# Kernel tuning notes

Measured on AMD Instinct MI355X. Metric: run time of the kernel, lower is better.

The kernel has to match this reference:

```python
import jax, jax.numpy as jnp
import numpy as np

DIM = 1024
RANK = 16
CLAMP = 5.0
PLASTICITY = 0.5
SING_THRESH = 0.8
SING_STRENGTH = 10.0


def setup_inputs() -> dict:
    key = jax.random.key(0)
    ks = jax.random.split(key, 8)
    B, S = 8, 4096
    v = jax.random.normal(ks[0], (B, S, DIM), dtype=jnp.float32)
    x = jax.random.normal(ks[1], (B, S, DIM), dtype=jnp.float32)
    U = jax.random.normal(ks[2], (DIM, RANK), dtype=jnp.float32) * 0.001
    W = jax.random.normal(ks[3], (DIM, RANK), dtype=jnp.float32) * 0.001
    # V: Linear(dim, 1, bias=False); init zeros in code, use small randn for coverage
    V_w = jax.random.normal(ks[4], (1, DIM), dtype=jnp.float32) * 0.01
    gate_w = jax.random.normal(ks[5], (DIM, DIM), dtype=jnp.float32) * 0.001
    gate_b = jnp.full((DIM,), 2.0, dtype=jnp.float32)
    forget_w = jax.random.normal(ks[6], (DIM, DIM), dtype=jnp.float32) * 0.01
    forget_b = jnp.full((DIM,), -3.0, dtype=jnp.float32)
    return {"v": v, "x": x, "U": U, "W": W, "V_w": V_w,
            "gate_w": gate_w, "gate_b": gate_b,
            "forget_w": forget_w, "forget_b": forget_b}


def reference(v, x, U, W, V_w, gate_w, gate_b, forget_w, forget_b):
    # Low-rank quadratic form: Gamma(v, v)
    proj = jnp.einsum('bsd,dr->bsr', v, U)                     # [B,S,R]
    norm = jnp.linalg.norm(proj, axis=-1, keepdims=True)       # [B,S,1]
    scale = 1.0 / (1.0 + norm)
    sq = proj * proj * scale                                   # [B,S,R]
    gamma = jnp.einsum('bsr,dr->bsd', sq, W)                   # [B,S,D]

    # Potential modulation (V has no bias)
    potential = jax.nn.sigmoid(jnp.einsum('bsd,od->bso', x, V_w))  # [B,S,1]
    gamma = gamma * (1.0 + potential)
    gamma = jnp.clip(gamma, -CLAMP, CLAMP)

    # Gate
    gate = jax.nn.sigmoid(jnp.einsum('bsd,ed->bse', x, gate_w) + gate_b)
    gamma = gamma * gate

    # Friction / damping
    friction = jax.nn.sigmoid(jnp.einsum('bsd,ed->bse', x, forget_w) + forget_b)
    out = gamma + friction * v

    # Reactive curvature (plasticity on kinetic energy)
    energy = jnp.tanh(jnp.mean(v * v, axis=-1, keepdims=True))
    out = out * (1.0 + PLASTICITY * energy)

    # Logical singularities (black holes)
    is_sing = (potential > SING_THRESH).astype(out.dtype)
    sing_mult = 1.0 + is_sing * (SING_STRENGTH - 1.0)
    out = out * sing_mult
    return out
```

## Files before the change

kernel.cpp:

```cpp
#include <hip/hip_runtime.h>
#include <hip/hip_fp16.h>
#include <math.h>


#define NROWS 32768
#define DIMD  1024

typedef float    f32x4 __attribute__((ext_vector_type(4)));
typedef _Float16 f16x8 __attribute__((ext_vector_type(8)));
typedef _Float16 f16x4 __attribute__((ext_vector_type(4)));

__global__ __launch_bounds__(256)
void k0_convert_w(const float* __restrict__ gw, const float* __restrict__ fw,
                  __half* __restrict__ wh) {
    const int NG = (2 * 1024 * 1024) / 4;
    for (int g = blockIdx.x * blockDim.x + threadIdx.x; g < NG; g += gridDim.x * blockDim.x) {
        int idx = g * 4;
        const float* src = (idx < 1024 * 1024) ? (gw + idx) : (fw + (idx - 1024 * 1024));
        f32x4 s = *(const f32x4*)src;
        f16x4 h;
        h[0] = (_Float16)s[0]; h[1] = (_Float16)s[1];
        h[2] = (_Float16)s[2]; h[3] = (_Float16)s[3];
        *(f16x4*)(wh + idx) = h;
    }
}

__global__ __launch_bounds__(256)
void k1_rowstats(const float* __restrict__ v, const float* __restrict__ x,
                 const float* __restrict__ U, const float* __restrict__ Vw,
                 float* __restrict__ sq_o, float* __restrict__ pot_o,
                 float* __restrict__ mult_o) {
    __shared__ float Us[1024][20];
    __shared__ float Vws[1024];
    const int tid = threadIdx.x;
    #pragma unroll
    for (int c = 0; c < 4; ++c) {
        int d = tid + 256 * c;
        const float* ur = U + (size_t)d * 16;
        *(f32x4*)&Us[d][0]  = *(const f32x4*)(ur);
        *(f32x4*)&Us[d][4]  = *(const f32x4*)(ur + 4);
        *(f32x4*)&Us[d][8]  = *(const f32x4*)(ur + 8);
        *(f32x4*)&Us[d][12] = *(const f32x4*)(ur + 12);
        Vws[d] = Vw[d];
    }
    __syncthreads();
    const int lane = tid & 63, wave = tid >> 6;
    const int gwv = blockIdx.x * 4 + wave;
    for (int rr = 0; rr < 8; ++rr) {
        int row = gwv + rr * 4096;
        const float* vr = v + (size_t)row * DIMD;
        const float* xr = x + (size_t)row * DIMD;
        float en = 0.f, pt = 0.f;
        float pr[16];
        #pragma unroll
        for (int r = 0; r < 16; ++r) pr[r] = 0.f;
        #pragma unroll 4
        for (int c = 0; c < 16; ++c) {
            int d = lane + 64 * c;
            float vv = vr[d];
            float xx = xr[d];
            en = fmaf(vv, vv, en);
            pt = fmaf(xx, Vws[d], pt);
            const float* up = &Us[d][0];
            #pragma unroll
            for (int r = 0; r < 16; ++r) pr[r] = fmaf(vv, up[r], pr[r]);
        }
        #pragma unroll
        for (int off = 32; off >= 1; off >>= 1) {
            en += __shfl_xor(en, off, 64);
            pt += __shfl_xor(pt, off, 64);
            #pragma unroll
            for (int r = 0; r < 16; ++r) pr[r] += __shfl_xor(pr[r], off, 64);
        }
        if (lane == 0) {
            float n2 = 0.f;
            #pragma unroll
            for (int r = 0; r < 16; ++r) n2 = fmaf(pr[r], pr[r], n2);
            float scale = 1.f / (1.f + sqrtf(n2));
            float p = 1.f / (1.f + expf(-pt));
            float energy = tanhf(en * (1.f / 1024.f));
            float mu = (1.f + 0.5f * energy) * (p > 0.8f ? 10.f : 1.f);
            float* sqr = sq_o + (size_t)row * 16;
            #pragma unroll
            for (int r = 0; r < 16; ++r) sqr[r] = pr[r] * pr[r] * scale;
            pot_o[row] = p;
            mult_o[row] = mu;
        }
    }
}

__global__ __launch_bounds__(256)
void k2_main(const float* __restrict__ x, const float* __restrict__ v,
             const __half* __restrict__ wh,
             const float* __restrict__ W, const float* __restrict__ gate_b,
             const float* __restrict__ forget_b, const float* __restrict__ sq_i,
             const float* __restrict__ pot_i, const float* __restrict__ mult_i,
             float* __restrict__ out) {
    __shared__ __half As[128][72];
    __shared__ __half Bs[2][64][64];
    __shared__ float  sqs[128][16];
    __shared__ float  Ws[64][20];
    __shared__ float  pots[128];
    __shared__ float  mults[128];
    __shared__ float  gbs[64];
    __shared__ float  fbs[64];

    const int tid  = threadIdx.x;
    const int lane = tid & 63, wave = tid >> 6;
    const int nt = blockIdx.x, mt = blockIdx.y;
    const int m0 = mt * 128, n0 = nt * 64;
    const int wm = (wave >> 1) * 64, wn = (wave & 1) * 32;

    {
        int r = tid >> 1, h = tid & 1;
        const float* s = sq_i + (size_t)(m0 + r) * 16 + h * 8;
        *(f32x4*)&sqs[r][h * 8]     = *(const f32x4*)(s);
        *(f32x4*)&sqs[r][h * 8 + 4] = *(const f32x4*)(s + 4);
        if (tid < 128) { pots[tid] = pot_i[m0 + tid]; mults[tid] = mult_i[m0 + tid]; }
        if (tid < 64)  { gbs[tid] = gate_b[n0 + tid]; fbs[tid] = forget_b[n0 + tid]; }
        int wr_ = tid >> 2, wq = tid & 3;
        *(f32x4*)&Ws[wr_][wq * 4] = *(const f32x4*)(W + (size_t)(n0 + wr_) * 16 + wq * 4);
    }

    f32x4 acc[2][4][2];
    #pragma unroll
    for (int a = 0; a < 2; ++a)
        #pragma unroll
        for (int m = 0; m < 4; ++m)
            #pragma unroll
            for (int n = 0; n < 2; ++n)
                acc[a][m][n] = (f32x4){0.f, 0.f, 0.f, 0.f};

    const int bn = lane >> 3;
    const int bs = (lane & 7) ^ bn;
    const int mat = wave >> 1;
    const __half* wsrc = wh + (size_t)(mat * 1024 + n0) * 1024;

    const int ar = tid >> 4;
    const int ac = tid & 15;
    const float* xbase = x + (size_t)(m0 + ar) * 1024 + ac * 4;

    for (int kt = 0; kt < 16; ++kt) {
        #pragma unroll
        for (int cc = 0; cc < 4; ++cc) {
            int c = (wave & 1) * 4 + cc;
            const __half* g = wsrc + (size_t)(c * 8 + bn) * 1024 + kt * 64 + bs * 8;
            __builtin_amdgcn_global_load_lds(
                (const __attribute__((address_space(1))) void*)g,
                (__attribute__((address_space(3))) void*)&Bs[mat][c * 8][0],
                16, 0, 0);
        }
        const float* xk = xbase + kt * 64;
        f32x4 xa[8];
        #pragma unroll
        for (int p = 0; p < 8; ++p) xa[p] = *(const f32x4*)(xk + (size_t)p * 16 * 1024);
        #pragma unroll
        for (int p = 0; p < 8; ++p) {
            f16x4 h;
            h[0] = (_Float16)xa[p][0]; h[1] = (_Float16)xa[p][1];
            h[2] = (_Float16)xa[p][2]; h[3] = (_Float16)xa[p][3];
            *(f16x4*)&As[p * 16 + ar][ac * 4] = h;
        }
        __syncthreads();

        #pragma unroll
        for (int kk = 0; kk < 2; ++kk) {
            f16x8 af[4];
            #pragma unroll
            for (int m = 0; m < 4; ++m) {
                int row = wm + m * 16 + (lane & 15);
                af[m] = *(const f16x8*)((const __half*)&As[row][0] + (lane >> 4) * 8 + kk * 32);
            }
            f16x8 bf[2][2];
            #pragma unroll
            for (int n = 0; n < 2; ++n) {
                int brow = wn + n * 16 + (lane & 15);
                int slot = ((lane >> 4) + kk * 4) ^ (brow & 7);
                bf[0][n] = *(const f16x8*)&Bs[0][brow][slot * 8];
                bf[1][n] = *(const f16x8*)&Bs[1][brow][slot * 8];
            }
            #pragma unroll
            for (int m = 0; m < 4; ++m)
                #pragma unroll
                for (int n = 0; n < 2; ++n) {
                    acc[0][m][n] = __builtin_amdgcn_mfma_f32_16x16x32_f16(af[m], bf[0][n], acc[0][m][n], 0, 0, 0);
                    acc[1][m][n] = __builtin_amdgcn_mfma_f32_16x16x32_f16(af[m], bf[1][n], acc[1][m][n], 0, 0, 0);
                }
        }
        __syncthreads();
    }

    const int cl = lane & 15;
    const int rq = lane >> 4;
    float gb2[2], fb2[2];
    f32x4 Wf[2][4];
    #pragma unroll
    for (int n = 0; n < 2; ++n) {
        int c = wn + n * 16 + cl;
        #pragma unroll
        for (int q = 0; q < 4; ++q) Wf[n][q] = *(const f32x4*)&Ws[c][q * 4];
        gb2[n] = gbs[c]; fb2[n] = fbs[c];
    }
    #pragma unroll
    for (int m = 0; m < 4; ++m) {
        #pragma unroll
        for (int i = 0; i < 4; ++i) {
            int rl = wm + m * 16 + rq * 4 + i;
            size_t gm = (size_t)(m0 + rl);
            f32x4 sr[4];
            #pragma unroll
            for (int q = 0; q < 4; ++q) sr[q] = *(const f32x4*)&sqs[rl][q * 4];
            float ptl = pots[rl], mu = mults[rl];
            float onep = 1.f + ptl;
            #pragma unroll
            for (int n = 0; n < 2; ++n) {
                float gamma = 0.f;
                #pragma unroll
                for (int q = 0; q < 4; ++q)
                    #pragma unroll
                    for (int j = 0; j < 4; ++j)
                        gamma = fmaf(sr[q][j], Wf[n][q][j], gamma);
                int gn = n0 + wn + n * 16 + cl;
                float gl = acc[0][m][n][i] + gb2[n];
                float fl = acc[1][m][n][i] + fb2[n];
                float gate = 1.f / (1.f + __expf(-gl));
                float fric = 1.f / (1.f + __expf(-fl));
                float gam = gamma * onep;
                gam = fminf(fmaxf(gam, -5.f), 5.f) * gate;
                float vv = v[gm * 1024 + gn];
                out[gm * 1024 + gn] = (gam + fric * vv) * mu;
            }
        }
    }
}

extern "C" void kernel_launch(void* const* d_in, const int* in_sizes, int n_in,
                              void* d_out, int out_size, void* d_ws, size_t ws_size,
                              hipStream_t stream) {
    const float* v  = (const float*)d_in[0];
    const float* x  = (const float*)d_in[1];
    const float* U  = (const float*)d_in[2];
    const float* W  = (const float*)d_in[3];
    const float* Vw = (const float*)d_in[4];
    const float* gw = (const float*)d_in[5];
    const float* gb = (const float*)d_in[6];
    const float* fw = (const float*)d_in[7];
    const float* fb = (const float*)d_in[8];
    float* out = (float*)d_out;

    __half* wh  = (__half*)d_ws;
    float* sq   = (float*)((char*)d_ws + (size_t)4 * 1024 * 1024);
    float* pot  = (float*)((char*)d_ws + (size_t)6 * 1024 * 1024);
    float* mult = (float*)((char*)d_ws + (size_t)6 * 1024 * 1024 + 131072);

    hipLaunchKernelGGL(k0_convert_w, dim3(1024), dim3(256), 0, stream, gw, fw, wh);
    hipLaunchKernelGGL(k1_rowstats,  dim3(1024), dim3(256), 0, stream, v, x, U, Vw, sq, pot, mult);
    hipLaunchKernelGGL(k2_main, dim3(16, 256), dim3(256), 0, stream,
                       x, v, wh, W, gb, fb, sq, pot, mult, out);
}
```

Baseline: 653.3 us.

## Pre-convert x to swizzled fp16 tiles, use MFMA for U projection, swizzle block order

Row-stats work is split into two kernels. One computes the potential from x and optionally writes x as pre-swizzled fp16 tiles. The other computes the v·U projection with MFMA against a transposed fp16 copy of U, replacing the scalar 16-way FMA and shuffle reductions. The main GEMM then streams A tiles straight into LDS with global_load_lds instead of reloading and converting fp32 x for each of the 16 column tiles, and uses an XOR-swizzled A layout plus a remapped block order for L2 locality. The cost is an extra fp16 copy of x written to workspace when it is large enough, an extra launch, and fp16 rounding in the low-rank projection.

```diff
diff --git a/kernel.cpp b/kernel.cpp
--- a/kernel.cpp
+++ b/kernel.cpp
@@ -2,19 +2,20 @@
 #include <hip/hip_fp16.h>
 #include <math.h>
 
-
-#define NROWS 32768
-#define DIMD  1024
-
 typedef float    f32x4 __attribute__((ext_vector_type(4)));
 typedef _Float16 f16x8 __attribute__((ext_vector_type(8)));
 typedef _Float16 f16x4 __attribute__((ext_vector_type(4)));
 
+#define AS1 __attribute__((address_space(1)))
+#define AS3 __attribute__((address_space(3)))
+
+
 __global__ __launch_bounds__(256)
-void k0_convert_w(const float* __restrict__ gw, const float* __restrict__ fw,
-                  __half* __restrict__ wh) {
+void k0_convert(const float* __restrict__ gw, const float* __restrict__ fw,
+                const float* __restrict__ U, _Float16* __restrict__ wh,
+                _Float16* __restrict__ uht) {
     const int NG = (2 * 1024 * 1024) / 4;
-    for (int g = blockIdx.x * blockDim.x + threadIdx.x; g < NG; g += gridDim.x * blockDim.x) {
+    for (int g = blockIdx.x * 256 + threadIdx.x; g < NG; g += gridDim.x * 256) {
         int idx = g * 4;
         const float* src = (idx < 1024 * 1024) ? (gw + idx) : (fw + (idx - 1024 * 1024));
         f32x4 s = *(const f32x4*)src;
@@ -23,81 +24,131 @@
         h[2] = (_Float16)s[2]; h[3] = (_Float16)s[3];
         *(f16x4*)(wh + idx) = h;
     }
-}
-
+    if (blockIdx.x < 64) {
+        int g = blockIdx.x * 256 + threadIdx.x;
+        int k = g >> 4, r = g & 15;
+        uht[r * 1032 + k] = (_Float16)U[k * 16 + r];
+    }
+}
+
+template<bool WRITE_XH>
 __global__ __launch_bounds__(256)
-void k1_rowstats(const float* __restrict__ v, const float* __restrict__ x,
-                 const float* __restrict__ U, const float* __restrict__ Vw,
-                 float* __restrict__ sq_o, float* __restrict__ pot_o,
-                 float* __restrict__ mult_o) {
-    __shared__ float Us[1024][20];
+void k0_x(const float* __restrict__ x, const float* __restrict__ Vw,
+          _Float16* __restrict__ xh, float* __restrict__ pot_o) {
     __shared__ float Vws[1024];
     const int tid = threadIdx.x;
     #pragma unroll
-    for (int c = 0; c < 4; ++c) {
-        int d = tid + 256 * c;
-        const float* ur = U + (size_t)d * 16;
-        *(f32x4*)&Us[d][0]  = *(const f32x4*)(ur);
-        *(f32x4*)&Us[d][4]  = *(const f32x4*)(ur + 4);
-        *(f32x4*)&Us[d][8]  = *(const f32x4*)(ur + 8);
-        *(f32x4*)&Us[d][12] = *(const f32x4*)(ur + 12);
-        Vws[d] = Vw[d];
-    }
+    for (int c = 0; c < 4; ++c) Vws[tid + 256 * c] = Vw[tid + 256 * c];
     __syncthreads();
-    const int lane = tid & 63, wave = tid >> 6;
-    const int gwv = blockIdx.x * 4 + wave;
-    for (int rr = 0; rr < 8; ++rr) {
-        int row = gwv + rr * 4096;
-        const float* vr = v + (size_t)row * DIMD;
-        const float* xr = x + (size_t)row * DIMD;
-        float en = 0.f, pt = 0.f;
-        float pr[16];
-        #pragma unroll
-        for (int r = 0; r < 16; ++r) pr[r] = 0.f;
-        #pragma unroll 4
-        for (int c = 0; c < 16; ++c) {
-            int d = lane + 64 * c;
-            float vv = vr[d];
-            float xx = xr[d];
-            en = fmaf(vv, vv, en);
-            pt = fmaf(xx, Vws[d], pt);
-            const float* up = &Us[d][0];
-            #pragma unroll
-            for (int r = 0; r < 16; ++r) pr[r] = fmaf(vv, up[r], pr[r]);
-        }
-        #pragma unroll
-        for (int off = 32; off >= 1; off >>= 1) {
-            en += __shfl_xor(en, off, 64);
-            pt += __shfl_xor(pt, off, 64);
-            #pragma unroll
-            for (int r = 0; r < 16; ++r) pr[r] += __shfl_xor(pr[r], off, 64);
-        }
-        if (lane == 0) {
-            float n2 = 0.f;
-            #pragma unroll
-            for (int r = 0; r < 16; ++r) n2 = fmaf(pr[r], pr[r], n2);
-            float scale = 1.f / (1.f + sqrtf(n2));
-            float p = 1.f / (1.f + expf(-pt));
-            float energy = tanhf(en * (1.f / 1024.f));
-            float mu = (1.f + 0.5f * energy) * (p > 0.8f ? 10.f : 1.f);
-            float* sqr = sq_o + (size_t)row * 16;
-            #pragma unroll
-            for (int r = 0; r < 16; ++r) sqr[r] = pr[r] * pr[r] * scale;
-            pot_o[row] = p;
-            mult_o[row] = mu;
-        }
-    }
-}
-
+    const int mt = blockIdx.x, m0 = mt * 128;
+    const int row = tid >> 1, half = tid & 1;
+    const float* xr = x + (size_t)(m0 + row) * 1024 + half * 32;
+    _Float16* xtile = xh + (size_t)mt * 16 * 128 * 64;
+    float pt = 0.f;
+    for (int kt = 0; kt < 16; ++kt) {
+        f32x4 a[8];
+        #pragma unroll
+        for (int j = 0; j < 8; ++j) a[j] = *(const f32x4*)(xr + kt * 64 + j * 4);
+        #pragma unroll
+        for (int j = 0; j < 8; ++j) {
+            const float* vw = &Vws[kt * 64 + half * 32 + j * 4];
+            pt = fmaf(a[j][0], vw[0], pt); pt = fmaf(a[j][1], vw[1], pt);
+            pt = fmaf(a[j][2], vw[2], pt); pt = fmaf(a[j][3], vw[3], pt);
+        }
+        if (WRITE_XH) {
+            _Float16* rowp = xtile + ((size_t)kt * 128 + row) * 64;
+            #pragma unroll
+            for (int jj = 0; jj < 4; ++jj) {
+                int slot = half * 4 + jj;
+                int phys = slot ^ (row & 7);
+                f16x8 h;
+                h[0] = (_Float16)a[2*jj][0];   h[1] = (_Float16)a[2*jj][1];
+                h[2] = (_Float16)a[2*jj][2];   h[3] = (_Float16)a[2*jj][3];
+                h[4] = (_Float16)a[2*jj+1][0]; h[5] = (_Float16)a[2*jj+1][1];
+                h[6] = (_Float16)a[2*jj+1][2]; h[7] = (_Float16)a[2*jj+1][3];
+                *(f16x8*)(rowp + phys * 8) = h;
+            }
+        }
+    }
+    pt += __shfl_xor(pt, 1, 64);
+    if (half == 0) pot_o[m0 + row] = 1.f / (1.f + expf(-pt));
+}
+
+__global__ __launch_bounds__(256)
+void k1_v(const float* __restrict__ v, const _Float16* __restrict__ uht,
+          const float* __restrict__ pot_i, float* __restrict__ sq_o,
+          float* __restrict__ mult_o) {
+    __shared__ _Float16 Av[64][64];
+    const int tid = threadIdx.x, lane = tid & 63, w = tid >> 6;
+    const int m0 = blockIdx.x * 64;
+    const int row = tid >> 2, q = tid & 3;
+    const float* vr = v + (size_t)(m0 + row) * 1024 + q * 16;
+    const _Float16* bsrc = uht + (lane & 15) * 1032 + (lane >> 4) * 8;
+    float en = 0.f;
+    f32x4 acc = {0.f, 0.f, 0.f, 0.f};
+    const int frow = w * 16 + (lane & 15);
+    for (int kt = 0; kt < 16; ++kt) {
+        f16x8 bf0 = *(const f16x8*)(bsrc + kt * 64);
+        f16x8 bf1 = *(const f16x8*)(bsrc + kt * 64 + 32);
+        f32x4 a[4];
+        #pragma unroll
+        for (int j = 0; j < 4; ++j) a[j] = *(const f32x4*)(vr + kt * 64 + j * 4);
+        #pragma unroll
+        for (int j = 0; j < 4; ++j) {
+            en = fmaf(a[j][0], a[j][0], en); en = fmaf(a[j][1], a[j][1], en);
+            en = fmaf(a[j][2], a[j][2], en); en = fmaf(a[j][3], a[j][3], en);
+        }
+        #pragma unroll
+        for (int jj = 0; jj < 2; ++jj) {
+            int slot = q * 2 + jj;
+            int phys = slot ^ (row & 7);
+            f16x8 h;
+            h[0] = (_Float16)a[2*jj][0];   h[1] = (_Float16)a[2*jj][1];
+            h[2] = (_Float16)a[2*jj][2];   h[3] = (_Float16)a[2*jj][3];
+            h[4] = (_Float16)a[2*jj+1][0]; h[5] = (_Float16)a[2*jj+1][1];
+            h[6] = (_Float16)a[2*jj+1][2]; h[7] = (_Float16)a[2*jj+1][3];
+            *(f16x8*)&Av[row][phys * 8] = h;
+        }
+        #pragma unroll
+        for (int kk = 0; kk < 2; ++kk) {
+            int lg = (lane >> 4) + kk * 4;
+            int phys = lg ^ (frow & 7);
+            f16x8 af = *(const f16x8*)&Av[frow][phys * 8];
+            acc = __builtin_amdgcn_mfma_f32_16x16x32_f16(af, kk ? bf1 : bf0, acc, 0, 0, 0);
+        }
+    }
+    const int r = lane & 15;
+    #pragma unroll
+    for (int i = 0; i < 4; ++i) {
+        float p2 = acc[i] * acc[i];
+        p2 += __shfl_xor(p2, 1, 64);
+        p2 += __shfl_xor(p2, 2, 64);
+        p2 += __shfl_xor(p2, 4, 64);
+        p2 += __shfl_xor(p2, 8, 64);
+        float scale = 1.f / (1.f + sqrtf(p2));
+        int prow = m0 + w * 16 + (lane >> 4) * 4 + i;
+        sq_o[(size_t)prow * 16 + r] = acc[i] * acc[i] * scale;
+    }
+    en += __shfl_xor(en, 1, 64);
+    en += __shfl_xor(en, 2, 64);
+    if (q == 0) {
+        int prow = m0 + row;
+        float e = tanhf(en * (1.f / 1024.f));
+        float p = pot_i[prow];
+        mult_o[prow] = (1.f + 0.5f * e) * (p > 0.8f ? 10.f : 1.f);
+    }
+}
+
+template<bool XH>
 __global__ __launch_bounds__(256)
 void k2_main(const float* __restrict__ x, const float* __restrict__ v,
-             const __half* __restrict__ wh,
+             const _Float16* __restrict__ wh, const _Float16* __restrict__ xh,
              const float* __restrict__ W, const float* __restrict__ gate_b,
              const float* __restrict__ forget_b, const float* __restrict__ sq_i,
              const float* __restrict__ pot_i, const float* __restrict__ mult_i,
              float* __restrict__ out) {
-    __shared__ __half As[128][72];
-    __shared__ __half Bs[2][64][64];
+    __shared__ _Float16 As[128][64];
+    __shared__ _Float16 Bs[2][64][64];
     __shared__ float  sqs[128][16];
     __shared__ float  Ws[64][20];
     __shared__ float  pots[128];
@@ -107,7 +158,9 @@
 
     const int tid  = threadIdx.x;
     const int lane = tid & 63, wave = tid >> 6;
-    const int nt = blockIdx.x, mt = blockIdx.y;
+    const int bid = blockIdx.x;
+    const int swz = (bid & 7) * 512 + (bid >> 3);
+    const int nt = swz & 15, mt = swz >> 4;
     const int m0 = mt * 128, n0 = nt * 64;
     const int wm = (wave >> 1) * 64, wn = (wave & 1) * 32;
 
@@ -134,32 +187,39 @@
     const int bn = lane >> 3;
     const int bs = (lane & 7) ^ bn;
     const int mat = wave >> 1;
-    const __half* wsrc = wh + (size_t)(mat * 1024 + n0) * 1024;
-
-    const int ar = tid >> 4;
-    const int ac = tid & 15;
-    const float* xbase = x + (size_t)(m0 + ar) * 1024 + ac * 4;
+    const _Float16* wsrc = wh + (size_t)(mat * 1024 + n0) * 1024;
+    const _Float16* xtile = XH ? (xh + (size_t)mt * 16 * 128 * 64) : nullptr;
+    const int ar = tid >> 4, ac = tid & 15;
+    const float* xbase = XH ? nullptr : (x + (size_t)(m0 + ar) * 1024 + ac * 4);
 
     for (int kt = 0; kt < 16; ++kt) {
         #pragma unroll
         for (int cc = 0; cc < 4; ++cc) {
             int c = (wave & 1) * 4 + cc;
-            const __half* g = wsrc + (size_t)(c * 8 + bn) * 1024 + kt * 64 + bs * 8;
-            __builtin_amdgcn_global_load_lds(
-                (const __attribute__((address_space(1))) void*)g,
-                (__attribute__((address_space(3))) void*)&Bs[mat][c * 8][0],
-                16, 0, 0);
-        }
-        const float* xk = xbase + kt * 64;
-        f32x4 xa[8];
-        #pragma unroll
-        for (int p = 0; p < 8; ++p) xa[p] = *(const f32x4*)(xk + (size_t)p * 16 * 1024);
-        #pragma unroll
-        for (int p = 0; p < 8; ++p) {
-            f16x4 h;
-            h[0] = (_Float16)xa[p][0]; h[1] = (_Float16)xa[p][1];
-            h[2] = (_Float16)xa[p][2]; h[3] = (_Float16)xa[p][3];
-            *(f16x4*)&As[p * 16 + ar][ac * 4] = h;
+            const _Float16* g = wsrc + (size_t)(c * 8 + bn) * 1024 + kt * 64 + bs * 8;
+            __builtin_amdgcn_global_load_lds((const AS1 void*)g,
+                (AS3 void*)&Bs[mat][c * 8][0], 16, 0, 0);
+        }
+        if (XH) {
+            const _Float16* xt = xtile + ((size_t)kt * 128) * 64;
+            #pragma unroll
+            for (int c = 0; c < 4; ++c) {
+                const _Float16* g = xt + (wave * 32 + c * 8) * 64 + lane * 8;
+                __builtin_amdgcn_global_load_lds((const AS1 void*)g,
+                    (AS3 void*)&As[wave * 32 + c * 8][0], 16, 0, 0);
+            }
+        } else {
+            const float* xk = xbase + kt * 64;
+            #pragma unroll
+            for (int p = 0; p < 8; ++p) {
+                f32x4 s = *(const f32x4*)(xk + (size_t)p * 16 * 1024);
+                f16x4 h;
+                h[0] = (_Float16)s[0]; h[1] = (_Float16)s[1];
+                h[2] = (_Float16)s[2]; h[3] = (_Float16)s[3];
+                int row = p * 16 + ar;
+                int phys = (ac >> 1) ^ (row & 7);
+                *(f16x4*)((_Float16*)&As[row][0] + phys * 8 + (ac & 1) * 4) = h;
+            }
         }
         __syncthreads();
 
@@ -169,7 +229,8 @@
             #pragma unroll
             for (int m = 0; m < 4; ++m) {
                 int row = wm + m * 16 + (lane & 15);
-                af[m] = *(const f16x8*)((const __half*)&As[row][0] + (lane >> 4) * 8 + kk * 32);
+                int phys = ((lane >> 4) + kk * 4) ^ (row & 7);
+                af[m] = *(const f16x8*)&As[row][phys * 8];
             }
             f16x8 bf[2][2];
             #pragma unroll
@@ -190,15 +251,14 @@
         __syncthreads();
     }
 
-    const int cl = lane & 15;
-    const int rq = lane >> 4;
+    const int cl = lane & 15, rq = lane >> 4;
     float gb2[2], fb2[2];
     f32x4 Wf[2][4];
     #pragma unroll
     for (int n = 0; n < 2; ++n) {
         int c = wn + n * 16 + cl;
         #pragma unroll
-        for (int q = 0; q < 4; ++q) Wf[n][q] = *(const f32x4*)&Ws[c][q * 4];
+        for (int qq = 0; qq < 4; ++qq) Wf[n][qq] = *(const f32x4*)&Ws[c][qq * 4];
         gb2[n] = gbs[c]; fb2[n] = fbs[c];
     }
     #pragma unroll
@@ -209,17 +269,16 @@
             size_t gm = (size_t)(m0 + rl);
             f32x4 sr[4];
             #pragma unroll
-            for (int q = 0; q < 4; ++q) sr[q] = *(const f32x4*)&sqs[rl][q * 4];
-            float ptl = pots[rl], mu = mults[rl];
-            float onep = 1.f + ptl;
+            for (int qq = 0; qq < 4; ++qq) sr[qq] = *(const f32x4*)&sqs[rl][qq * 4];
+            float onep = 1.f + pots[rl], mu = mults[rl];
             #pragma unroll
             for (int n = 0; n < 2; ++n) {
                 float gamma = 0.f;
                 #pragma unroll
-                for (int q = 0; q < 4; ++q)
+                for (int qq = 0; qq < 4; ++qq)
                     #pragma unroll
                     for (int j = 0; j < 4; ++j)
-                        gamma = fmaf(sr[q][j], Wf[n][q][j], gamma);
+                        gamma = fmaf(sr[qq][j], Wf[n][qq][j], gamma);
                 int gn = n0 + wn + n * 16 + cl;
                 float gl = acc[0][m][n][i] + gb2[n];
                 float fl = acc[1][m][n][i] + fb2[n];
@@ -248,13 +307,21 @@
     const float* fb = (const float*)d_in[8];
     float* out = (float*)d_out;
 
-    __half* wh  = (__half*)d_ws;
-    float* sq   = (float*)((char*)d_ws + (size_t)4 * 1024 * 1024);
-    float* pot  = (float*)((char*)d_ws + (size_t)6 * 1024 * 1024);
-    float* mult = (float*)((char*)d_ws + (size_t)6 * 1024 * 1024 + 131072);
-
-    hipLaunchKernelGGL(k0_convert_w, dim3(1024), dim3(256), 0, stream, gw, fw, wh);
-    hipLaunchKernelGGL(k1_rowstats,  dim3(1024), dim3(256), 0, stream, v, x, U, Vw, sq, pot, mult);
-    hipLaunchKernelGGL(k2_main, dim3(16, 256), dim3(256), 0, stream,
-                       x, v, wh, W, gb, fb, sq, pot, mult, out);
-}
+    const size_t MB = 1024 * 1024;
+    _Float16* wh  = (_Float16*)d_ws;
+    _Float16* uht = (_Float16*)((char*)d_ws + 4 * MB);
+    float* sq     = (float*)((char*)d_ws + 4 * MB + 65536);
+    float* pot    = (float*)((char*)d_ws + 6 * MB + 65536);
+    float* mult   = (float*)((char*)d_ws + 6 * MB + 65536 + 131072);
+    _Float16* xh  = (_Float16*)((char*)d_ws + 8 * MB);
+    const bool big = ws_size >= 72 * MB;
+
+    hipLaunchKernelGGL(k0_convert, dim3(1024), dim3(256), 0, stream, gw, fw, U, wh, uht);
+    if (big) hipLaunchKernelGGL(k0_x<true>,  dim3(256), dim3(256), 0, stream, x, Vw, xh, pot);
+    else     hipLaunchKernelGGL(k0_x<false>, dim3(256), dim3(256), 0, stream, x, Vw, xh, pot);
+    hipLaunchKernelGGL(k1_v, dim3(512), dim3(256), 0, stream, v, uht, pot, sq, mult);
+    if (big) hipLaunchKernelGGL(k2_main<true>,  dim3(4096), dim3(256), 0, stream,
+                                x, v, wh, xh, W, gb, fb, sq, pot, mult, out);
+    else     hipLaunchKernelGGL(k2_main<false>, dim3(4096), dim3(256), 0, stream,
+                                x, v, wh, xh, W, gb, fb, sq, pot, mult, out);
+}
```

Result: faster. 591.0 us (-9.5%).
